# Kernel optimization log

Hardware: AMD Instinct MI355X
Metric: run time of the kernel (lower is better)

## Reference

```python
import jax, jax.numpy as jnp
import numpy as np

N, D = 16384, 16     # nodes (hits), node feature dim (= embedding dim, slice is full)
K = 64               # max_num_neighbors
MAX_RADIUS = 6.0     # kNN radius cut
PID_MAX = 5000


def setup_inputs() -> dict:
    key = jax.random.key(0)
    k1, k2 = jax.random.split(key)
    x = jax.random.normal(k1, (N, D), dtype=jnp.float32)
    particle_id = jax.random.randint(k2, (N,), 0, PID_MAX, dtype=jnp.int32)
    return {"x": x, "particle_id": particle_id}


def reference(x, particle_id):
    # ml is None and embedding_slice=(None,None) -> embedding features are x itself
    emb = x
    # knn_graph: squared pairwise distances, self-loops excluded (diag = +inf)
    sq = jnp.sum(emb * emb, axis=1)                       # [N]
    d2 = sq[:, None] + sq[None, :] - 2.0 * (emb @ emb.T)  # [N, N]
    diag = jnp.arange(N)
    d2 = d2.at[diag, diag].set(jnp.inf)
    _, nbr = jax.lax.top_k(-d2, K)                        # [N, K] nearest neighbor ids
    src = nbr.reshape(-1)                                 # edge_index[0]: neighbor (source)
    dst = jnp.repeat(jnp.arange(N, dtype=src.dtype), K)   # edge_index[1]: query node
    # radius filter: keep edges with dist < max_radius (fixed shape -> boolean mask)
    diff = x[src] - x[dst]                                # [N*K, D]
    dists = jnp.sqrt(jnp.maximum(jnp.sum(diff * diff, axis=1), 0.0))
    mask = dists < MAX_RADIUS                             # [N*K]
    # edge truth labels: same (nonzero) particle id on both ends
    y = (particle_id[src] == particle_id[dst]) & (particle_id[src] > 0) & mask
    # edge features: [x_src - x_dst, x_src + x_dst], zeroed on masked-out edges
    edge_features = jnp.concatenate([diff, x[src] + x[dst]], axis=1)
    edge_features = edge_features * mask[:, None].astype(x.dtype)
    edge_index = jnp.stack([src, dst])                    # [2, N*K]
    return x, edge_index, y.astype(jnp.int32), edge_features, mask
```

## Files before the change

kernel.cpp:

```cpp
#include <hip/hip_runtime.h>

#define NN 16384
#define DD 16
#define KK 64
#define QQ 4
#define TPB 256
#define NCHUNK 8
#define HIST 1024
#define HISTW (HIST/2)
#define LIST_MAX 768
#define CAND_MAX 256

__device__ __forceinline__ float halving_sumsq16(const float* v) {
    float p[16];
#pragma unroll
    for (int d = 0; d < 16; ++d) p[d] = __fmul_rn(v[d], v[d]);
    float r8[8];
#pragma unroll
    for (int j = 0; j < 8; ++j) r8[j] = __fadd_rn(p[j], p[j + 8]);
    float r4[4];
#pragma unroll
    for (int j = 0; j < 4; ++j) r4[j] = __fadd_rn(r8[j], r8[j + 4]);
    float r2[2];
#pragma unroll
    for (int j = 0; j < 2; ++j) r2[j] = __fadd_rn(r4[j], r4[j + 2]);
    return __fadd_rn(r2[0], r2[1]);
}

__device__ __forceinline__ float d2_of(const float* xi, const float* xj,
                                       float sqi, float sqj) {
    float dot = 0.0f;
#pragma unroll
    for (int d = 0; d < DD; ++d) dot = fmaf(xi[d], xj[d], dot);
    return __fsub_rn(__fadd_rn(sqi, sqj), __fmul_rn(2.0f, dot));
}

__device__ __forceinline__ int bucket_of(float d2) {
    int b = (int)__fmul_rn(d2, 4.0f);
    if (b < 0) b = 0;
    if (b >= HIST) b = HIST - 1;
    return b;
}

#define LOAD_XQ()                                                              \
    float xq[QQ][DD];                                                          \
    float sq[QQ], Tq[QQ];                                                      \
    _Pragma("unroll") for (int q = 0; q < QQ; ++q) {                           \
        const float4* p = reinterpret_cast<const float4*>(x + (iA + q) * DD);  \
        float4 a0 = p[0], a1 = p[1], a2 = p[2], a3 = p[3];                     \
        xq[q][0]=a0.x; xq[q][1]=a0.y; xq[q][2]=a0.z; xq[q][3]=a0.w;            \
        xq[q][4]=a1.x; xq[q][5]=a1.y; xq[q][6]=a1.z; xq[q][7]=a1.w;            \
        xq[q][8]=a2.x; xq[q][9]=a2.y; xq[q][10]=a2.z; xq[q][11]=a2.w;          \
        xq[q][12]=a3.x; xq[q][13]=a3.y; xq[q][14]=a3.z; xq[q][15]=a3.w;        \
        sq[q] = sqf[iA + q];                                                   \
        Tq[q] = 16.0f + sq[q] - 1.8f * sqrtf(32.0f + 4.0f * sq[q]);            \
    }

#define LOAD_XJ(j)                                                             \
    const float4* xj4 = reinterpret_cast<const float4*>(x + (j) * DD);         \
    float4 a0 = xj4[0], a1 = xj4[1], a2 = xj4[2], a3 = xj4[3];                 \
    float xj[DD] = {a0.x, a0.y, a0.z, a0.w, a1.x, a1.y, a1.z, a1.w,            \
                    a2.x, a2.y, a2.z, a2.w, a3.x, a3.y, a3.z, a3.w};

__global__ void prep_kernel(const float* __restrict__ x,
                            float* __restrict__ out_x,
                            float* __restrict__ sqf) {
    int i = blockIdx.x * blockDim.x + threadIdx.x;
    if (i < NN) {
        float v[DD];
#pragma unroll
        for (int d = 0; d < DD; ++d) v[d] = x[i * DD + d];
        sqf[i] = halving_sumsq16(v);
    }
    for (int t = i; t < NN * DD; t += gridDim.x * blockDim.x) {
        out_x[t] = x[t];
    }
}

__global__ __launch_bounds__(TPB, 4) void scan_kernel(
        const float* __restrict__ x,
        const float* __restrict__ sqf,
        unsigned int* __restrict__ ws_cnt,
        unsigned short* __restrict__ ws_list) {
    __shared__ unsigned int bm[NCHUNK][TPB];
    __shared__ unsigned short list[QQ][LIST_MAX];
    __shared__ unsigned int wcnt[TPB / 64][QQ];
    __shared__ unsigned int s_listcnt[QQ];

    const int bid = blockIdx.x;
    const int tid = threadIdx.x;
    const int lane = tid & 63;
    const int w = tid >> 6;
    const int iA = bid * QQ;

    LOAD_XQ();

#pragma unroll 1
    for (int c = 0; c < NCHUNK; ++c) {
        unsigned int bits = 0;
#pragma unroll
        for (int k = 0; k < 8; ++k) {
            const int j = (c * 8 + k) * TPB + tid;
            LOAD_XJ(j);
            const float sj = sqf[j];
#pragma unroll
            for (int q = 0; q < QQ; ++q) {
                float d2 = d2_of(xq[q], xj, sq[q], sj);
                if (d2 < Tq[q]) bits |= (1u << (4 * k + q));
            }
        }
        bm[c][tid] = bits;
    }
    __syncthreads();

    {
        unsigned int cnt[QQ] = {0, 0, 0, 0};
#pragma unroll 1
        for (int c = 0; c < NCHUNK; ++c) {
            unsigned int w32 = bm[c][tid];
#pragma unroll
            for (int q = 0; q < QQ; ++q)
                cnt[q] += (unsigned int)__popc(w32 & (0x11111111u << q));
        }
        unsigned int excl[QQ];
#pragma unroll
        for (int q = 0; q < QQ; ++q) {
            unsigned int v = cnt[q];
#pragma unroll
            for (int off = 1; off < 64; off <<= 1) {
                unsigned int n = __shfl_up(v, off, 64);
                if (lane >= off) v += n;
            }
            excl[q] = v - cnt[q];
            if (lane == 63) wcnt[w][q] = v;
        }
        __syncthreads();
        if (tid < QQ)
            s_listcnt[tid] = wcnt[0][tid] + wcnt[1][tid] + wcnt[2][tid] + wcnt[3][tid];
        unsigned int cur[QQ];
#pragma unroll
        for (int q = 0; q < QQ; ++q) {
            unsigned int b = 0;
            for (int ww = 0; ww < w; ++ww) b += wcnt[ww][q];
            cur[q] = b + excl[q];
        }
#pragma unroll 1
        for (int c = 0; c < NCHUNK; ++c) {
            unsigned int t32 = bm[c][tid];
            while (t32) {
                int b = __ffs(t32) - 1;
                int q = b & 3;
                int k = b >> 2;
                unsigned int pos = cur[q]++;
                if (pos < LIST_MAX)
                    list[q][pos] = (unsigned short)((c * 8 + k) * TPB + tid);
                t32 &= t32 - 1;
            }
        }
    }
    __syncthreads();

    for (int q = 0; q < QQ; ++q) {
        int lc = (int)min(s_listcnt[q], (unsigned int)LIST_MAX);
        unsigned short* dst = ws_list + ((long)iA + q) * LIST_MAX;
        for (int e = tid; e < lc; e += TPB) dst[e] = list[q][e];
    }
    if (tid < QQ) ws_cnt[iA + tid] = s_listcnt[tid];
}

__global__ __launch_bounds__(TPB) void select_kernel(
        const float* __restrict__ x,
        const int* __restrict__ pid,
        const float* __restrict__ sqf,
        const unsigned int* __restrict__ ws_cnt,
        const unsigned short* __restrict__ ws_list,
        float* __restrict__ out_src,
        float* __restrict__ out_dst,
        float* __restrict__ out_y,
        float* __restrict__ out_ef,
        float* __restrict__ out_mask) {
    __shared__ unsigned short list[QQ][LIST_MAX];
    __shared__ unsigned int hist[QQ][HISTW];
    __shared__ unsigned int cand_key[QQ][CAND_MAX];
    __shared__ int cand_idx[QQ][CAND_MAX];
    __shared__ unsigned int wavesum[QQ][TPB / 64];
    __shared__ int s_bsel[QQ];
    __shared__ unsigned int s_excnt[QQ], s_candcnt[QQ], s_lc[QQ];
    __shared__ int s_fb[QQ];

    const int bid = blockIdx.x;
    const int tid = threadIdx.x;
    const int lane = tid & 63;
    const int w = tid >> 6;
    const int iA = bid * QQ;

    for (int t = tid; t < QQ * HISTW; t += TPB)
        ((unsigned int*)hist)[t] = 0;
    if (tid < QQ) {
        s_excnt[tid] = 0; s_candcnt[tid] = 0; s_bsel[tid] = HIST - 1;
        s_lc[tid] = min(ws_cnt[iA + tid], (unsigned int)LIST_MAX);
    }
    LOAD_XQ();
    __syncthreads();

    for (int q = 0; q < QQ; ++q) {
        const unsigned short* src = ws_list + ((long)iA + q) * LIST_MAX;
        const int lc = (int)s_lc[q];
        for (int e = tid; e < lc; e += TPB) list[q][e] = src[e];
    }
    __syncthreads();

    for (int q = 0; q < QQ; ++q) {
        const int lc = (int)s_lc[q];
        unsigned int my = 0;
        for (int e = tid; e < lc; e += TPB) {
            const int j = list[q][e];
            LOAD_XJ(j);
            float d2 = d2_of(xq[q], xj, sq[q], sqf[j]);
            my += (d2 < Tq[q]) ? 1u : 0u;
            int b = bucket_of(d2);
            atomicAdd(&hist[q][b >> 1], 1u << ((b & 1) << 4));
        }
        unsigned int v = my;
#pragma unroll
        for (int off = 1; off < 64; off <<= 1) v += __shfl_xor(v, off, 64);
        if (lane == 0 && v) atomicAdd(&s_excnt[q], v);
    }
    __syncthreads();

    if (tid < QQ)
        s_fb[tid] = (ws_cnt[iA + tid] > LIST_MAX) || (s_excnt[tid] < KK + 1);
    __syncthreads();
    const int anyfb = s_fb[0] | s_fb[1] | s_fb[2] | s_fb[3];

    if (anyfb) {
#pragma unroll
        for (int q = 0; q < QQ; ++q)
            if (s_fb[q])
                for (int t = tid; t < HISTW; t += TPB) hist[q][t] = 0;
        __syncthreads();
        for (int j = tid; j < NN; j += TPB) {
            LOAD_XJ(j);
            const float sj = sqf[j];
#pragma unroll
            for (int q = 0; q < QQ; ++q) {
                if (s_fb[q] && j != iA + q) {
                    float d2 = d2_of(xq[q], xj, sq[q], sj);
                    int b = bucket_of(d2);
                    atomicAdd(&hist[q][b >> 1], 1u << ((b & 1) << 4));
                }
            }
        }
    }
    __syncthreads();

    {
        unsigned int local[QQ], inc[QQ];
        unsigned int pc0[QQ], pc1[QQ], pc2[QQ], pc3[QQ];
#pragma unroll
        for (int q = 0; q < QQ; ++q) {
            unsigned int h0 = hist[q][2 * tid];
            unsigned int h1 = hist[q][2 * tid + 1];
            pc0[q] = h0 & 0xFFFFu; pc1[q] = h0 >> 16;
            pc2[q] = h1 & 0xFFFFu; pc3[q] = h1 >> 16;
            unsigned int s = pc0[q] + pc1[q] + pc2[q] + pc3[q];
            local[q] = s;
            unsigned int v = s;
#pragma unroll
            for (int off = 1; off < 64; off <<= 1) {
                unsigned int n = __shfl_up(v, off, 64);
                if (lane >= off) v += n;
            }
            inc[q] = v;
        }
        if (lane == 63)
#pragma unroll
            for (int q = 0; q < QQ; ++q) wavesum[q][w] = inc[q];
        __syncthreads();
#pragma unroll
        for (int q = 0; q < QQ; ++q) {
            const unsigned int need = s_fb[q] ? KK : (KK + 1);
            unsigned int woff = 0;
            for (int ww = 0; ww < w; ++ww) woff += wavesum[q][ww];
            unsigned int cum = inc[q] + woff;
            unsigned int prev = cum - local[q];
            if (prev < need && need <= cum) {
                unsigned int acc = prev;
                int b = 4 * tid;
                if (acc + pc0[q] < need) { acc += pc0[q]; ++b;
                    if (acc + pc1[q] < need) { acc += pc1[q]; ++b;
                        if (acc + pc2[q] < need) { acc += pc2[q]; ++b; } } }
                s_bsel[q] = b;
            }
        }
    }
    __syncthreads();

#pragma unroll
    for (int q = 0; q < QQ; ++q) {
        if (!s_fb[q]) {
            const int bsel = s_bsel[q];
            const int lc = (int)s_lc[q];
            for (int e = tid; e < lc; e += TPB) {
                const int j = list[q][e];
                LOAD_XJ(j);
                float d2 = d2_of(xq[q], xj, sq[q], sqf[j]);
                if (bucket_of(d2) <= bsel && j != iA + q) {
                    unsigned int pos = atomicAdd(&s_candcnt[q], 1u);
                    if (pos < CAND_MAX) {
                        unsigned int u = __float_as_uint(d2);
                        u ^= (u & 0x80000000u) ? 0xFFFFFFFFu : 0x80000000u;
                        cand_key[q][pos] = u;
                        cand_idx[q][pos] = j;
                    }
                }
            }
        }
    }
    if (anyfb) {
        for (int j = tid; j < NN; j += TPB) {
            LOAD_XJ(j);
            const float sj = sqf[j];
#pragma unroll
            for (int q = 0; q < QQ; ++q) {
                if (s_fb[q] && j != iA + q) {
                    float d2 = d2_of(xq[q], xj, sq[q], sj);
                    if (bucket_of(d2) <= s_bsel[q]) {
                        unsigned int pos = atomicAdd(&s_candcnt[q], 1u);
                        if (pos < CAND_MAX) {
                            unsigned int u = __float_as_uint(d2);
                            u ^= (u & 0x80000000u) ? 0xFFFFFFFFu : 0x80000000u;
                            cand_key[q][pos] = u;
                            cand_idx[q][pos] = j;
                        }
                    }
                }
            }
        }
    }
    __syncthreads();

    for (int q = 0; q < QQ; ++q) {
        const int iq = iA + q;
        const int mypid = pid[iq];
        int c = (int)s_candcnt[q];
        if (c > CAND_MAX) c = CAND_MAX;
        for (int t = tid; t < c; t += TPB) {
            const unsigned int kt = cand_key[q][t];
            const int jt = cand_idx[q][t];
            int rank = 0;
            for (int u = 0; u < c; ++u) {
                unsigned int ku = cand_key[q][u];
                rank += (ku < kt) || (ku == kt && cand_idx[q][u] < jt);
            }
            if (rank < KK) {
                const long e = (long)iq * KK + rank;
                out_src[e] = (float)jt;

                const float* xjp = x + jt * DD;
                float diff[DD], sum[DD];
#pragma unroll
                for (int d = 0; d < DD; ++d) {
                    float a = xjp[d], b = xq[q][d];
                    diff[d] = __fsub_rn(a, b);
                    sum[d]  = __fadd_rn(a, b);
                }
                const float s2 = halving_sumsq16(diff);
                const bool m = __fsqrt_rn(s2) < 6.0f;
                out_mask[e] = m ? 1.0f : 0.0f;
                const int pj = pid[jt];
                out_y[e] = (m && pj == mypid && pj > 0) ? 1.0f : 0.0f;

                float* ef = out_ef + e * (2 * DD);
#pragma unroll
                for (int d = 0; d < DD; ++d) ef[d] = m ? diff[d] : 0.0f;
#pragma unroll
                for (int d = 0; d < DD; ++d) ef[DD + d] = m ? sum[d] : 0.0f;
            }
        }
    }

    for (int t = tid; t < QQ * KK; t += TPB) {
        out_dst[(long)iA * KK + t] = (float)(iA + t / KK);
    }
}

extern "C" void kernel_launch(void* const* d_in, const int* in_sizes, int n_in,
                              void* d_out, int out_size, void* d_ws, size_t ws_size,
                              hipStream_t stream) {
    const float* x = (const float*)d_in[0];
    const int* pid = (const int*)d_in[1];
    float* out = (float*)d_out;

    float* out_x   = out;
    float* out_src = out_x + NN * DD;
    float* out_dst = out_src + NN * KK;
    float* out_y   = out_dst + NN * KK;
    float* out_ef  = out_y + NN * KK;
    float* out_mask = out_ef + (long)NN * KK * 2 * DD;

    float* sqf = (float*)d_ws;
    unsigned int* ws_cnt = (unsigned int*)((char*)d_ws + NN * sizeof(float));
    unsigned short* ws_list =
        (unsigned short*)((char*)d_ws + NN * sizeof(float) + NN * sizeof(unsigned int));

    prep_kernel<<<NN / 256, 256, 0, stream>>>(x, out_x, sqf);
    scan_kernel<<<NN / QQ, TPB, 0, stream>>>(x, sqf, ws_cnt, ws_list);
    select_kernel<<<NN / QQ, TPB, 0, stream>>>(x, pid, sqf, ws_cnt, ws_list,
                                               out_src, out_dst, out_y,
                                               out_ef, out_mask);
}
```

Measured before the change: 425.9 us.

## Scan candidates from transposed x with float4 per-thread column blocks

The prep kernel now also writes a feature-major transposed copy of x to workspace. Each scan thread handles four consecutive candidates per chunk, loading float4 columns from the transpose and accumulating dot products with FMAs, then forming d2 as sq_i + sq_j - 2*dot instead of calling the earlier d2 helper. The bitmask becomes 16-bit per chunk, and the launch-bounds occupancy hint rises from 4 to 6. The candidate ordering in the lists changes and the d2 arithmetic differs from the previous helper, so the threshold filter's rounding may differ slightly.

```diff
diff --git a/kernel.cpp b/kernel.cpp
--- a/kernel.cpp
+++ b/kernel.cpp
@@ -5,7 +5,7 @@
 #define KK 64
 #define QQ 4
 #define TPB 256
-#define NCHUNK 8
+#define NQW 16
 #define HIST 1024
 #define HISTW (HIST/2)
 #define LIST_MAX 768
@@ -64,25 +64,29 @@
 
 __global__ void prep_kernel(const float* __restrict__ x,
                             float* __restrict__ out_x,
-                            float* __restrict__ sqf) {
+                            float* __restrict__ sqf,
+                            float* __restrict__ xt) {
     int i = blockIdx.x * blockDim.x + threadIdx.x;
     if (i < NN) {
         float v[DD];
 #pragma unroll
         for (int d = 0; d < DD; ++d) v[d] = x[i * DD + d];
         sqf[i] = halving_sumsq16(v);
+#pragma unroll
+        for (int d = 0; d < DD; ++d) xt[d * NN + i] = v[d];
     }
     for (int t = i; t < NN * DD; t += gridDim.x * blockDim.x) {
         out_x[t] = x[t];
     }
 }
 
-__global__ __launch_bounds__(TPB, 4) void scan_kernel(
+__global__ __launch_bounds__(TPB, 6) void scan_kernel(
         const float* __restrict__ x,
+        const float* __restrict__ xt,
         const float* __restrict__ sqf,
         unsigned int* __restrict__ ws_cnt,
         unsigned short* __restrict__ ws_list) {
-    __shared__ unsigned int bm[NCHUNK][TPB];
+    __shared__ unsigned short bm[NQW][TPB];
     __shared__ unsigned short list[QQ][LIST_MAX];
     __shared__ unsigned int wcnt[TPB / 64][QQ];
     __shared__ unsigned int s_listcnt[QQ];
@@ -96,31 +100,47 @@
     LOAD_XQ();
 
 #pragma unroll 1
-    for (int c = 0; c < NCHUNK; ++c) {
+    for (int c = 0; c < NQW; ++c) {
+        const int qd = c * TPB + tid;
+        float4 sjv = reinterpret_cast<const float4*>(sqf)[qd];
+        float4 acc[QQ];
+#pragma unroll
+        for (int q = 0; q < QQ; ++q) acc[q] = make_float4(0.f, 0.f, 0.f, 0.f);
+#pragma unroll
+        for (int d = 0; d < DD; ++d) {
+            float4 xv = reinterpret_cast<const float4*>(xt + (long)d * NN)[qd];
+#pragma unroll
+            for (int q = 0; q < QQ; ++q) {
+                acc[q].x = fmaf(xq[q][d], xv.x, acc[q].x);
+                acc[q].y = fmaf(xq[q][d], xv.y, acc[q].y);
+                acc[q].z = fmaf(xq[q][d], xv.z, acc[q].z);
+                acc[q].w = fmaf(xq[q][d], xv.w, acc[q].w);
+            }
+        }
         unsigned int bits = 0;
 #pragma unroll
-        for (int k = 0; k < 8; ++k) {
-            const int j = (c * 8 + k) * TPB + tid;
-            LOAD_XJ(j);
-            const float sj = sqf[j];
-#pragma unroll
-            for (int q = 0; q < QQ; ++q) {
-                float d2 = d2_of(xq[q], xj, sq[q], sj);
-                if (d2 < Tq[q]) bits |= (1u << (4 * k + q));
-            }
-        }
-        bm[c][tid] = bits;
+        for (int q = 0; q < QQ; ++q) {
+            float d2x = __fsub_rn(__fadd_rn(sq[q], sjv.x), __fmul_rn(2.0f, acc[q].x));
+            float d2y = __fsub_rn(__fadd_rn(sq[q], sjv.y), __fmul_rn(2.0f, acc[q].y));
+            float d2z = __fsub_rn(__fadd_rn(sq[q], sjv.z), __fmul_rn(2.0f, acc[q].z));
+            float d2w = __fsub_rn(__fadd_rn(sq[q], sjv.w), __fmul_rn(2.0f, acc[q].w));
+            if (d2x < Tq[q]) bits |= (1u << (0 * 4 + q));
+            if (d2y < Tq[q]) bits |= (1u << (1 * 4 + q));
+            if (d2z < Tq[q]) bits |= (1u << (2 * 4 + q));
+            if (d2w < Tq[q]) bits |= (1u << (3 * 4 + q));
+        }
+        bm[c][tid] = (unsigned short)bits;
     }
     __syncthreads();
 
     {
         unsigned int cnt[QQ] = {0, 0, 0, 0};
 #pragma unroll 1
-        for (int c = 0; c < NCHUNK; ++c) {
-            unsigned int w32 = bm[c][tid];
+        for (int c = 0; c < NQW; ++c) {
+            unsigned int w16 = bm[c][tid];
 #pragma unroll
             for (int q = 0; q < QQ; ++q)
-                cnt[q] += (unsigned int)__popc(w32 & (0x11111111u << q));
+                cnt[q] += (unsigned int)__popc(w16 & (0x1111u << q));
         }
         unsigned int excl[QQ];
 #pragma unroll
@@ -145,16 +165,16 @@
             cur[q] = b + excl[q];
         }
 #pragma unroll 1
-        for (int c = 0; c < NCHUNK; ++c) {
-            unsigned int t32 = bm[c][tid];
-            while (t32) {
-                int b = __ffs(t32) - 1;
+        for (int c = 0; c < NQW; ++c) {
+            unsigned int t16 = bm[c][tid];
+            while (t16) {
+                int b = __ffs(t16) - 1;
                 int q = b & 3;
-                int k = b >> 2;
+                int jl = b >> 2;
                 unsigned int pos = cur[q]++;
                 if (pos < LIST_MAX)
-                    list[q][pos] = (unsigned short)((c * 8 + k) * TPB + tid);
-                t32 &= t32 - 1;
+                    list[q][pos] = (unsigned short)((c * TPB + tid) * 4 + jl);
+                t16 &= t16 - 1;
             }
         }
     }
@@ -399,13 +419,15 @@
     float* out_ef  = out_y + NN * KK;
     float* out_mask = out_ef + (long)NN * KK * 2 * DD;
 
-    float* sqf = (float*)d_ws;
-    unsigned int* ws_cnt = (unsigned int*)((char*)d_ws + NN * sizeof(float));
+    char* wsb = (char*)d_ws;
+    float* sqf = (float*)wsb;
+    float* xt = (float*)(wsb + (long)NN * 4);
+    unsigned int* ws_cnt = (unsigned int*)(wsb + (long)NN * 4 + (long)NN * DD * 4);
     unsigned short* ws_list =
-        (unsigned short*)((char*)d_ws + NN * sizeof(float) + NN * sizeof(unsigned int));
-
-    prep_kernel<<<NN / 256, 256, 0, stream>>>(x, out_x, sqf);
-    scan_kernel<<<NN / QQ, TPB, 0, stream>>>(x, sqf, ws_cnt, ws_list);
+        (unsigned short*)(wsb + (long)NN * 4 + (long)NN * DD * 4 + (long)NN * 4);
+
+    prep_kernel<<<NN / 256, 256, 0, stream>>>(x, out_x, sqf, xt);
+    scan_kernel<<<NN / QQ, TPB, 0, stream>>>(x, xt, sqf, ws_cnt, ws_list);
     select_kernel<<<NN / QQ, TPB, 0, stream>>>(x, pid, sqf, ws_cnt, ws_list,
                                                out_src, out_dst, out_y,
                                                out_ef, out_mask);
```

Result: faster. 374.9 us (-12.0%).
